# Kernel tuning notes

Hardware: AMD Instinct MI355X
Metric: run time of the kernel (lower is better)

## Reference

```python
import jax, jax.numpy as jnp
import numpy as np

B, S, D, F, E, SH, K = 2, 2048, 2048, 1024, 16, 2, 2


def setup_inputs() -> dict:
    key = jax.random.key(0)
    ks = jax.random.split(key, 8)
    std = 0.02
    mk = lambda k, sh: (jax.random.normal(k, sh, jnp.float32) * std)
    return {
        "x": jax.random.normal(ks[0], (B, S, D), jnp.float32),
        "wa": mk(ks[1], (D, E)),                      # router, no bias
        "rg": mk(ks[2], (E, D, F)), "rgb": jnp.zeros((E, F), jnp.float32),
        "rw1": mk(ks[3], (E, D, F)), "rb1": jnp.zeros((E, F), jnp.float32),
        "rw2": mk(ks[4], (E, F, D)), "rb2": jnp.zeros((E, D), jnp.float32),
        "sg": mk(ks[5], (SH, D, F)), "sgb": jnp.zeros((SH, F), jnp.float32),
        "sw1": mk(ks[6], (SH, D, F)), "sb1": jnp.zeros((SH, F), jnp.float32),
        "sw2": mk(ks[7], (SH, F, D)), "sb2": jnp.zeros((SH, D), jnp.float32),
    }


def _experts_all(x, g, gb, w1, b1, w2, b2):
    """Run every expert in the stack on every token.
    x: [b,s,d]; g,w1: [e,d,f]; w2: [e,f,d] -> out [b,s,e,d].
    Expert: w2( gelu(gated(x)) * w1(x) ). torch GELU default = exact erf.
    """
    y = jax.nn.gelu(jnp.einsum('bsd,edf->bsef', x, g) + gb, approximate=False)
    y = y * (jnp.einsum('bsd,edf->bsef', x, w1) + b1)
    return jnp.einsum('bsef,efd->bsed', y, w2) + b2


def reference(x, wa, rg, rgb, rw1, rb1, rw2, rb2, sg, sgb, sw1, sb1, sw2, sb2):
    # sigmoid affinity router + top-k, renormalized over the k selected
    aff = jax.nn.sigmoid(jnp.einsum('bsd,de->bse', x, wa))
    topk_p, topk_i = jax.lax.top_k(aff, K)                   # [b,s,k]
    topk_p = topk_p / jnp.sum(topk_p, axis=-1, keepdims=True)
    # dense combine weights [b,s,E]; zero for unselected experts, so the
    # masked-scatter of the original is reproduced exactly by a weighted sum
    combine = jnp.sum(jax.nn.one_hot(topk_i, E, dtype=x.dtype) * topk_p[..., None], axis=2)
    routed = jnp.einsum('bsed,bse->bsd',
                        _experts_all(x, rg, rgb, rw1, rb1, rw2, rb2), combine)
    shared = jnp.sum(_experts_all(x, sg, sgb, sw1, sb1, sw2, sb2), axis=2)
    return x + shared + routed
```

## Files before the change

kernel.cpp:

```cpp
#include <hip/hip_runtime.h>
#include <hip/hip_bf16.h>
#include <math.h>

typedef __bf16 bf16;
typedef bf16  bf16x8 __attribute__((ext_vector_type(8)));
typedef bf16  bf16x4 __attribute__((ext_vector_type(4)));
typedef float f32x4  __attribute__((ext_vector_type(4)));

#define TOKENS 4096
#define DM 2048
#define FF 1024
#define NE 16
#define SH_BASE 12288
#define BK 64

#define WS_CNT    0
#define WS_POS    64
#define WS_BASE   128
#define WS_TOPKW  256
#define WS_TOPKI  33024
#define WS_TSLOT  65792
#define WS_LIST   98560
#define WS_XB     180480
#define WS_H      16957696
#define WS_Y      58900736
#define WS_B1R    142786816
#define WS_B1S    277004544
#define WS_W2TR   293781760
#define WS_W2TS   360890624

__device__ __forceinline__ bf16 f2bf(float f) {
  unsigned u = __builtin_bit_cast(unsigned, f);
  u += 0x7fffu + ((u >> 16) & 1u);
  unsigned short h = (unsigned short)(u >> 16);
  return __builtin_bit_cast(bf16, h);
}

typedef const __attribute__((address_space(1))) void* gas_t;
typedef __attribute__((address_space(3))) void* las_t;
__device__ __forceinline__ void load_lds16(const bf16* g, bf16* l) {
  __builtin_amdgcn_global_load_lds((gas_t)g, (las_t)l, 16, 0, 0);
}

__global__ void cvt_x_kernel(const float* __restrict__ x, bf16* __restrict__ xb) {
  const size_t idx = ((size_t)blockIdx.x * 256 + threadIdx.x) * 4;
  f32x4 v = *(const f32x4*)(x + idx);
  bf16x4 o;
  o[0] = f2bf(v[0]); o[1] = f2bf(v[1]); o[2] = f2bf(v[2]); o[3] = f2bf(v[3]);
  *(bf16x4*)(xb + idx) = o;
}

__global__ void transpose_cvt_kernel(const float* __restrict__ in, bf16* __restrict__ out,
                                     int R, int C) {
  __shared__ float tile[64][65];
  const size_t zo = (size_t)blockIdx.z * R * C;
  const int c0 = blockIdx.x * 64, r0 = blockIdx.y * 64;
  const int t = threadIdx.x;
  const int tc = t & 63, tr = t >> 6;
#pragma unroll
  for (int i = 0; i < 16; i++) {
    const int r = tr * 16 + i;
    tile[r][tc] = in[zo + (size_t)(r0 + r) * C + c0 + tc];
  }
  __syncthreads();
  const int co = t >> 4;
  const int ro = (t & 15) * 4;
#pragma unroll
  for (int j = 0; j < 4; j++) {
    const int c = co + j * 16;
    bf16x4 v;
    v[0] = f2bf(tile[ro + 0][c]);
    v[1] = f2bf(tile[ro + 1][c]);
    v[2] = f2bf(tile[ro + 2][c]);
    v[3] = f2bf(tile[ro + 3][c]);
    *(bf16x4*)(out + zo + (size_t)(c0 + c) * R + r0 + ro) = v;
  }
}

__global__ void transpose_cvt_fused_kernel(const float* __restrict__ in, bf16* __restrict__ out,
                                           int half) {
  __shared__ float tile[64][65];
  const size_t zi = (size_t)blockIdx.z * DM * FF;
  const size_t zo = (size_t)blockIdx.z * (2 * FF) * DM;
  const int c0 = blockIdx.x * 64, r0 = blockIdx.y * 64;
  const int t = threadIdx.x;
  const int tc = t & 63, tr = t >> 6;
#pragma unroll
  for (int i = 0; i < 16; i++) {
    const int r = tr * 16 + i;
    tile[r][tc] = in[zi + (size_t)(r0 + r) * FF + c0 + tc];
  }
  __syncthreads();
  const int co = t >> 4;
  const int ro = (t & 15) * 4;
#pragma unroll
  for (int j = 0; j < 4; j++) {
    const int c = co + j * 16;
    const int f = c0 + c;
    const int fr = ((f >> 4) << 5) + half * 16 + (f & 15);
    bf16x4 v;
    v[0] = f2bf(tile[ro + 0][c]);
    v[1] = f2bf(tile[ro + 1][c]);
    v[2] = f2bf(tile[ro + 2][c]);
    v[3] = f2bf(tile[ro + 3][c]);
    *(bf16x4*)(out + zo + (size_t)fr * DM + r0 + ro) = v;
  }
}

#define RT_TOK 16
#define RT_DK  256
#define RT_PITCH (RT_DK + 4)

__global__ __launch_bounds__(256) void router_kernel(
    const float* __restrict__ x, const float* __restrict__ wa,
    float* __restrict__ topk_w, int* __restrict__ topk_i,
    int* __restrict__ cnt) {
  __shared__ float xs[RT_TOK][RT_PITCH];
  __shared__ float was[NE][RT_PITCH];
  __shared__ float aff[RT_TOK][17];

  const int tid = threadIdx.x;
  const int t = tid >> 4;
  const int e = tid & 15;
  const int t0 = blockIdx.x * RT_TOK;

  f32x4 acc4 = {0.f, 0.f, 0.f, 0.f};

  for (int d0 = 0; d0 < DM; d0 += RT_DK) {
    __syncthreads();
    {
      const int r = tid >> 4;
      const int c4 = (tid & 15) * 4;
      const float* src = x + (size_t)(t0 + r) * DM + d0;
#pragma unroll
      for (int j = 0; j < 4; j++)
        *(f32x4*)(&xs[r][c4 + j * 64]) = *(const f32x4*)(src + c4 + j * 64);
    }
    {
      const int e2 = tid & 15;
      const int dd = (tid >> 4) * 16;
#pragma unroll
      for (int j = 0; j < 16; j++)
        was[e2][dd + j] = wa[(size_t)(d0 + dd + j) * NE + e2];
    }
    __syncthreads();
#pragma unroll 16
    for (int d = 0; d < RT_DK; d += 4) {
      const f32x4 xv = *(const f32x4*)(&xs[t][d]);
      const f32x4 wv = *(const f32x4*)(&was[e][d]);
      acc4 += xv * wv;
    }
  }

  const float a = acc4[0] + acc4[1] + acc4[2] + acc4[3];
  aff[t][e] = 1.f / (1.f + expf(-a));
  __syncthreads();

  if (e == 0) {
    float b0 = -1e30f, b1 = -1e30f; int i0 = 0, i1 = 0;
    for (int i = 0; i < NE; i++) {
      const float v = aff[t][i];
      if (v > b0) { b1 = b0; i1 = i0; b0 = v; i0 = i; }
      else if (v > b1) { b1 = v; i1 = i; }
    }
    const int tok = t0 + t;
    const float inv = 1.f / (b0 + b1);
    topk_w[tok * 2] = b0 * inv;  topk_w[tok * 2 + 1] = b1 * inv;
    topk_i[tok * 2] = i0;        topk_i[tok * 2 + 1] = i1;
    atomicAdd(&cnt[i0], 1);      atomicAdd(&cnt[i1], 1);
  }
}

__global__ void prefix_kernel(const int* __restrict__ cnt, int* __restrict__ base) {
  if (threadIdx.x == 0) {
    int acc = 0;
    for (int e = 0; e < NE; e++) { base[e] = acc; acc += (cnt[e] + 127) & ~127; }
    base[NE] = SH_BASE;
    base[NE + 1] = SH_BASE + TOKENS;
  }
}

__global__ void build_lists_kernel(const int* __restrict__ topk_i, const int* __restrict__ base,
                                   int* __restrict__ pos, int* __restrict__ list,
                                   int* __restrict__ token_slot) {
  const int t = blockIdx.x * 256 + threadIdx.x;
  if (t >= TOKENS) return;
#pragma unroll
  for (int k = 0; k < 2; k++) {
    const int e = topk_i[t * 2 + k];
    const int p = atomicAdd(&pos[e], 1);
    const int slot = base[e] + p;
    list[slot] = t;
    token_slot[t * 2 + k] = slot;
  }
  list[SH_BASE + t] = t;
  list[SH_BASE + TOKENS + t] = t;
}

__global__ __launch_bounds__(256, 2) void gemm1_kernel(
    const bf16* __restrict__ xb, const int* __restrict__ list,
    const int* __restrict__ base, const int* __restrict__ cnt,
    const bf16* __restrict__ B1R, const bf16* __restrict__ B1S,
    const float* __restrict__ rgb, const float* __restrict__ rb1,
    const float* __restrict__ sgb, const float* __restrict__ sb1,
    bf16* __restrict__ H) {
  const int e = blockIdx.z;
  const int ce = (e < NE) ? cnt[e] : TOKENS;
  const int m0 = blockIdx.y * 128;
  if (m0 >= ce) return;
  const int n0 = blockIdx.x * 128;
  const int bse = base[e];

  const bf16* B1; const float *gb, *ub;
  if (e < NE) { B1 = B1R + (size_t)e * (2 * FF) * DM; gb = rgb + e * FF; ub = rb1 + e * FF; }
  else { const int s = e - NE; B1 = B1S + (size_t)s * (2 * FF) * DM; gb = sgb + s * FF; ub = sb1 + s * FF; }

  __shared__ bf16 As[2][128 * BK];
  __shared__ bf16 Bs[2][128 * BK];

  const int tid = threadIdx.x, lane = tid & 63, wid = tid >> 6;
  const int lrow = lane >> 3;
  const int laneK = (((lane & 7) ^ lrow) << 3);
  const int q0 = wid << 5;

  const bf16* aP[4];
#pragma unroll
  for (int i = 0; i < 4; i++) {
    int rA = m0 + q0 + (i << 3) + lrow;
    if (rA >= ce) rA = ce - 1;
    aP[i] = xb + (size_t)list[bse + rA] * DM + laneK;
  }
  const bf16* bP = B1 + (size_t)(n0 + q0 + lrow) * DM + laneK;

  const int wm = (wid & 1) * 64, wn = (wid >> 1) * 64;
  const int m16 = lane & 15, quad = lane >> 4, xor7 = m16 & 7;

  f32x4 acc[4][4] = {};

#pragma unroll
  for (int i = 0; i < 4; i++) {
    load_lds16(aP[i], &As[0][(q0 + (i << 3)) * BK + (lane << 3)]);
    load_lds16(bP + (size_t)(i * 8) * DM, &Bs[0][(q0 + (i << 3)) * BK + (lane << 3)]);
  }

  int cur = 0;
  for (int k0 = 0; k0 < DM; k0 += BK) {
    __syncthreads();
    if (k0 + BK < DM) {
      const int nxt = cur ^ 1;
      const int kn = k0 + BK;
#pragma unroll
      for (int i = 0; i < 4; i++) {
        load_lds16(aP[i] + kn, &As[nxt][(q0 + (i << 3)) * BK + (lane << 3)]);
        load_lds16(bP + (size_t)(i * 8) * DM + kn, &Bs[nxt][(q0 + (i << 3)) * BK + (lane << 3)]);
      }
    }
#pragma unroll
    for (int kk = 0; kk < 2; kk++) {
      const int slot = (((kk << 2) + quad) ^ xor7) << 3;
      bf16x8 af[4], bfr[4];
#pragma unroll
      for (int i = 0; i < 4; i++) {
        af[i]  = *(const bf16x8*)(&As[cur][(wm + m16 + 16 * i) * BK + slot]);
        bfr[i] = *(const bf16x8*)(&Bs[cur][(wn + m16 + 16 * i) * BK + slot]);
      }
#pragma unroll
      for (int mi = 0; mi < 4; mi++)
#pragma unroll
        for (int ni = 0; ni < 4; ni++)
          acc[mi][ni] = __builtin_amdgcn_mfma_f32_16x16x32_bf16(af[mi], bfr[ni], acc[mi][ni], 0, 0, 0);
    }
    cur ^= 1;
  }

  const int q4 = quad * 4;
  const int fbase = ((n0 + wn) >> 1) + m16;
#pragma unroll
  for (int mi = 0; mi < 4; mi++) {
#pragma unroll
    for (int nj = 0; nj < 2; nj++) {
      const int f = fbase + nj * 16;
      const float gbv = gb[f], ubv = ub[f];
#pragma unroll
      for (int r = 0; r < 4; r++) {
        const int row = m0 + wm + mi * 16 + q4 + r;
        const float g = acc[mi][2 * nj][r] + gbv;
        const float u = acc[mi][2 * nj + 1][r] + ubv;
        const float h = 0.5f * g * (1.f + erff(g * 0.70710678118f)) * u;
        H[(size_t)(bse + row) * FF + f] = f2bf(h);
      }
    }
  }
}

__global__ __launch_bounds__(256, 2) void gemm2_kernel(
    const bf16* __restrict__ Hb, const int* __restrict__ base, const int* __restrict__ cnt,
    const bf16* __restrict__ rw2T, const bf16* __restrict__ sw2T,
    const float* __restrict__ rb2, const float* __restrict__ sb2,
    bf16* __restrict__ Y) {
  const int e = blockIdx.z;
  const int ce = (e < NE) ? cnt[e] : TOKENS;
  const int m0 = blockIdx.y * 128;
  if (m0 >= ce) return;
  const int n0 = blockIdx.x * 128;
  const int bse = base[e];

  const bf16* B; const float* bb;
  if (e < NE) { B = rw2T + (size_t)e * DM * FF; bb = rb2 + e * DM; }
  else { const int s = e - NE; B = sw2T + (size_t)s * DM * FF; bb = sb2 + s * DM; }

  __shared__ bf16 As[2][128 * BK];
  __shared__ bf16 Bs[2][128 * BK];

  const int tid = threadIdx.x, lane = tid & 63, wid = tid >> 6;
  const int lrow = lane >> 3;
  const int laneK = (((lane & 7) ^ lrow) << 3);
  const int q0 = wid << 5;

  const bf16* aP = Hb + (size_t)(bse + m0 + q0 + lrow) * FF + laneK;
  const bf16* bP = B  + (size_t)(n0 + q0 + lrow) * FF + laneK;

  const int wm = (wid & 1) * 64, wn = (wid >> 1) * 64;
  const int m16 = lane & 15, quad = lane >> 4, xor7 = m16 & 7;

  f32x4 acc[4][4] = {};

#pragma unroll
  for (int i = 0; i < 4; i++) {
    load_lds16(aP + (size_t)(i * 8) * FF, &As[0][(q0 + (i << 3)) * BK + (lane << 3)]);
    load_lds16(bP + (size_t)(i * 8) * FF, &Bs[0][(q0 + (i << 3)) * BK + (lane << 3)]);
  }

  int cur = 0;
  for (int k0 = 0; k0 < FF; k0 += BK) {
    __syncthreads();
    if (k0 + BK < FF) {
      const int nxt = cur ^ 1;
      const int kn = k0 + BK;
#pragma unroll
      for (int i = 0; i < 4; i++) {
        load_lds16(aP + (size_t)(i * 8) * FF + kn, &As[nxt][(q0 + (i << 3)) * BK + (lane << 3)]);
        load_lds16(bP + (size_t)(i * 8) * FF + kn, &Bs[nxt][(q0 + (i << 3)) * BK + (lane << 3)]);
      }
    }
#pragma unroll
    for (int kk = 0; kk < 2; kk++) {
      const int slot = (((kk << 2) + quad) ^ xor7) << 3;
      bf16x8 af[4], bfr[4];
#pragma unroll
      for (int i = 0; i < 4; i++) {
        af[i]  = *(const bf16x8*)(&As[cur][(wm + m16 + 16 * i) * BK + slot]);
        bfr[i] = *(const bf16x8*)(&Bs[cur][(wn + m16 + 16 * i) * BK + slot]);
      }
#pragma unroll
      for (int mi = 0; mi < 4; mi++)
#pragma unroll
        for (int ni = 0; ni < 4; ni++)
          acc[mi][ni] = __builtin_amdgcn_mfma_f32_16x16x32_bf16(af[mi], bfr[ni], acc[mi][ni], 0, 0, 0);
    }
    cur ^= 1;
  }

  const int q4 = quad * 4;
#pragma unroll
  for (int mi = 0; mi < 4; mi++) {
#pragma unroll
    for (int ni = 0; ni < 4; ni++) {
      const int n = n0 + wn + ni * 16 + m16;
      const float bv = bb[n];
#pragma unroll
      for (int r = 0; r < 4; r++) {
        const int row = m0 + wm + mi * 16 + q4 + r;
        Y[(size_t)(bse + row) * DM + n] = f2bf(acc[mi][ni][r] + bv);
      }
    }
  }
}

__global__ void combine_kernel(const float* __restrict__ x, const bf16* __restrict__ Y,
                               const int* __restrict__ token_slot, const float* __restrict__ topk_w,
                               float* __restrict__ out) {
  const int t = blockIdx.x;
  const int d = threadIdx.x * 8;
  const int s0 = token_slot[t * 2], s1 = token_slot[t * 2 + 1];
  const float w0 = topk_w[t * 2], w1 = topk_w[t * 2 + 1];
  const bf16x8 ya = *(const bf16x8*)(Y + (size_t)(SH_BASE + t) * DM + d);
  const bf16x8 yb = *(const bf16x8*)(Y + (size_t)(SH_BASE + TOKENS + t) * DM + d);
  const bf16x8 y0 = *(const bf16x8*)(Y + (size_t)s0 * DM + d);
  const bf16x8 y1 = *(const bf16x8*)(Y + (size_t)s1 * DM + d);
  const float* xp = x + (size_t)t * DM + d;
  float* op = out + (size_t)t * DM + d;
#pragma unroll
  for (int j = 0; j < 8; j++)
    op[j] = xp[j] + (float)ya[j] + (float)yb[j] + w0 * (float)y0[j] + w1 * (float)y1[j];
}

extern "C" void kernel_launch(void* const* d_in, const int* in_sizes, int n_in,
                              void* d_out, int out_size, void* d_ws, size_t ws_size,
                              hipStream_t stream) {
  (void)in_sizes; (void)n_in; (void)out_size; (void)ws_size;
  const float* x   = (const float*)d_in[0];
  const float* wa  = (const float*)d_in[1];
  const float* rg  = (const float*)d_in[2];
  const float* rgb = (const float*)d_in[3];
  const float* rw1 = (const float*)d_in[4];
  const float* rb1 = (const float*)d_in[5];
  const float* rw2 = (const float*)d_in[6];
  const float* rb2 = (const float*)d_in[7];
  const float* sg  = (const float*)d_in[8];
  const float* sgb = (const float*)d_in[9];
  const float* sw1 = (const float*)d_in[10];
  const float* sb1 = (const float*)d_in[11];
  const float* sw2 = (const float*)d_in[12];
  const float* sb2 = (const float*)d_in[13];
  float* out = (float*)d_out;

  char* ws = (char*)d_ws;
  int*   cnt        = (int*)(ws + WS_CNT);
  int*   pos        = (int*)(ws + WS_POS);
  int*   basep      = (int*)(ws + WS_BASE);
  float* topk_w     = (float*)(ws + WS_TOPKW);
  int*   topk_i     = (int*)(ws + WS_TOPKI);
  int*   token_slot = (int*)(ws + WS_TSLOT);
  int*   list       = (int*)(ws + WS_LIST);
  bf16*  xb         = (bf16*)(ws + WS_XB);
  bf16*  H          = (bf16*)(ws + WS_H);
  bf16*  Y          = (bf16*)(ws + WS_Y);
  bf16*  B1R        = (bf16*)(ws + WS_B1R);
  bf16*  B1S        = (bf16*)(ws + WS_B1S);
  bf16*  W2TR       = (bf16*)(ws + WS_W2TR);
  bf16*  W2TS       = (bf16*)(ws + WS_W2TS);

  hipMemsetAsync(ws, 0, 128, stream);

  cvt_x_kernel<<<(TOKENS * DM) / 1024, 256, 0, stream>>>(x, xb);
  router_kernel<<<TOKENS / RT_TOK, 256, 0, stream>>>(x, wa, topk_w, topk_i, cnt);
  prefix_kernel<<<1, 64, 0, stream>>>(cnt, basep);
  build_lists_kernel<<<TOKENS / 256, 256, 0, stream>>>(topk_i, basep, pos, list, token_slot);

  transpose_cvt_fused_kernel<<<dim3(FF / 64, DM / 64, NE), 256, 0, stream>>>(rg,  B1R, 0);
  transpose_cvt_fused_kernel<<<dim3(FF / 64, DM / 64, NE), 256, 0, stream>>>(rw1, B1R, 1);
  transpose_cvt_fused_kernel<<<dim3(FF / 64, DM / 64, 2),  256, 0, stream>>>(sg,  B1S, 0);
  transpose_cvt_fused_kernel<<<dim3(FF / 64, DM / 64, 2),  256, 0, stream>>>(sw1, B1S, 1);
  transpose_cvt_kernel<<<dim3(DM / 64, FF / 64, NE), 256, 0, stream>>>(rw2, W2TR, FF, DM);
  transpose_cvt_kernel<<<dim3(DM / 64, FF / 64, 2),  256, 0, stream>>>(sw2, W2TS, FF, DM);

  gemm1_kernel<<<dim3((2 * FF) / 128, 32, 18), 256, 0, stream>>>(
      xb, list, basep, cnt, B1R, B1S, rgb, rb1, sgb, sb1, H);
  gemm2_kernel<<<dim3(DM / 128, 32, 18), 256, 0, stream>>>(
      H, basep, cnt, W2TR, W2TS, rb2, sb2, Y);
  combine_kernel<<<TOKENS, 256, 0, stream>>>(x, Y, token_slot, topk_w, out);
}
```

Baseline: 916.5 us.

## Enlarge expert GEMM tiles to 256x256 with four-stage LDS pipeline

Both grouped expert GEMMs move from 128x128 tiles with a double-buffered K=64 loop to 256x256 tiles over 512 threads. The K loop now uses K=32 steps with a four-buffer LDS ring, explicit vmcnt waits and raw barriers, plus s_setprio around the MFMA block. Expert slot padding grows to 256 rows to match the new M tile. The aim is more operand reuse per loaded byte and better hiding of load latency. In exchange, each block needs 128KB of LDS, so only one block fits per CU, and the larger tiles waste more work on partially filled expert tiles.

```diff
diff --git a/kernel.cpp b/kernel.cpp
--- a/kernel.cpp
+++ b/kernel.cpp
@@ -12,7 +12,6 @@
 #define FF 1024
 #define NE 16
 #define SH_BASE 12288
-#define BK 64
 
 #define WS_CNT    0
 #define WS_POS    64
@@ -174,7 +173,7 @@
 __global__ void prefix_kernel(const int* __restrict__ cnt, int* __restrict__ base) {
   if (threadIdx.x == 0) {
     int acc = 0;
-    for (int e = 0; e < NE; e++) { base[e] = acc; acc += (cnt[e] + 127) & ~127; }
+    for (int e = 0; e < NE; e++) { base[e] = acc; acc += (cnt[e] + 255) & ~255; }
     base[NE] = SH_BASE;
     base[NE + 1] = SH_BASE + TOKENS;
   }
@@ -197,7 +196,8 @@
   list[SH_BASE + TOKENS + t] = t;
 }
 
-__global__ __launch_bounds__(256, 2) void gemm1_kernel(
+
+__global__ __launch_bounds__(512, 2) void gemm1_kernel(
     const bf16* __restrict__ xb, const int* __restrict__ list,
     const int* __restrict__ base, const int* __restrict__ cnt,
     const bf16* __restrict__ B1R, const bf16* __restrict__ B1S,
@@ -206,77 +206,85 @@
     bf16* __restrict__ H) {
   const int e = blockIdx.z;
   const int ce = (e < NE) ? cnt[e] : TOKENS;
-  const int m0 = blockIdx.y * 128;
+  const int m0 = blockIdx.y * 256;
   if (m0 >= ce) return;
-  const int n0 = blockIdx.x * 128;
+  const int n0 = blockIdx.x * 256;
   const int bse = base[e];
 
   const bf16* B1; const float *gb, *ub;
   if (e < NE) { B1 = B1R + (size_t)e * (2 * FF) * DM; gb = rgb + e * FF; ub = rb1 + e * FF; }
   else { const int s = e - NE; B1 = B1S + (size_t)s * (2 * FF) * DM; gb = sgb + s * FF; ub = sb1 + s * FF; }
 
-  __shared__ bf16 As[2][128 * BK];
-  __shared__ bf16 Bs[2][128 * BK];
+  __shared__ bf16 As[4 * 8192];
+  __shared__ bf16 Bs[4 * 8192];
 
   const int tid = threadIdx.x, lane = tid & 63, wid = tid >> 6;
-  const int lrow = lane >> 3;
-  const int laneK = (((lane & 7) ^ lrow) << 3);
-  const int q0 = wid << 5;
-
-  const bf16* aP[4];
-#pragma unroll
-  for (int i = 0; i < 4; i++) {
-    int rA = m0 + q0 + (i << 3) + lrow;
-    if (rA >= ce) rA = ce - 1;
-    aP[i] = xb + (size_t)list[bse + rA] * DM + laneK;
-  }
-  const bf16* bP = B1 + (size_t)(n0 + q0 + lrow) * DM + laneK;
-
-  const int wm = (wid & 1) * 64, wn = (wid >> 1) * 64;
-  const int m16 = lane & 15, quad = lane >> 4, xor7 = m16 & 7;
-
-  f32x4 acc[4][4] = {};
-
-#pragma unroll
-  for (int i = 0; i < 4; i++) {
-    load_lds16(aP[i], &As[0][(q0 + (i << 3)) * BK + (lane << 3)]);
-    load_lds16(bP + (size_t)(i * 8) * DM, &Bs[0][(q0 + (i << 3)) * BK + (lane << 3)]);
-  }
-
-  int cur = 0;
-  for (int k0 = 0; k0 < DM; k0 += BK) {
-    __syncthreads();
-    if (k0 + BK < DM) {
-      const int nxt = cur ^ 1;
-      const int kn = k0 + BK;
-#pragma unroll
-      for (int i = 0; i < 4; i++) {
-        load_lds16(aP[i] + kn, &As[nxt][(q0 + (i << 3)) * BK + (lane << 3)]);
-        load_lds16(bP + (size_t)(i * 8) * DM + kn, &Bs[nxt][(q0 + (i << 3)) * BK + (lane << 3)]);
-      }
-    }
-#pragma unroll
-    for (int kk = 0; kk < 2; kk++) {
-      const int slot = (((kk << 2) + quad) ^ xor7) << 3;
-      bf16x8 af[4], bfr[4];
-#pragma unroll
-      for (int i = 0; i < 4; i++) {
-        af[i]  = *(const bf16x8*)(&As[cur][(wm + m16 + 16 * i) * BK + slot]);
-        bfr[i] = *(const bf16x8*)(&Bs[cur][(wn + m16 + 16 * i) * BK + slot]);
-      }
-#pragma unroll
-      for (int mi = 0; mi < 4; mi++)
-#pragma unroll
-        for (int ni = 0; ni < 4; ni++)
-          acc[mi][ni] = __builtin_amdgcn_mfma_f32_16x16x32_bf16(af[mi], bfr[ni], acc[mi][ni], 0, 0, 0);
-    }
-    cur ^= 1;
+  const int m16 = lane & 15, quad = lane >> 4;
+  const int wm = (wid & 1) * 128, wn = (wid >> 1) * 64;
+  const int rg8 = (quad ^ (m16 & 3)) << 3;
+
+  const int r0 = tid >> 2;
+  const int swz = ((tid & 3) ^ (r0 & 3)) << 3;
+  int ra0 = m0 + r0;       if (ra0 >= ce) ra0 = ce - 1;
+  int ra1 = m0 + 128 + r0; if (ra1 >= ce) ra1 = ce - 1;
+  const bf16* aSrc0 = xb + (size_t)list[bse + ra0] * DM + swz;
+  const bf16* aSrc1 = xb + (size_t)list[bse + ra1] * DM + swz;
+  const bf16* bSrc0 = B1 + (size_t)(n0 + r0) * DM + swz;
+  const bf16* bSrc1 = B1 + (size_t)(n0 + 128 + r0) * DM + swz;
+
+  f32x4 acc[8][4] = {};
+
+#pragma unroll
+  for (int t = 0; t < 3; t++) {
+    bf16* Ad = As + t * 8192; bf16* Bd = Bs + t * 8192;
+    const int k = t * 32;
+    load_lds16(aSrc0 + k, Ad + tid * 8);
+    load_lds16(aSrc1 + k, Ad + 4096 + tid * 8);
+    load_lds16(bSrc0 + k, Bd + tid * 8);
+    load_lds16(bSrc1 + k, Bd + 4096 + tid * 8);
+  }
+  asm volatile("s_waitcnt vmcnt(8)" ::: "memory");
+  __builtin_amdgcn_s_barrier();
+
+  const int NT = DM / 32;
+  for (int t = 0; t < NT; ++t) {
+    if (t + 3 < NT) {
+      const int sb = (t + 3) & 3;
+      bf16* Ad = As + sb * 8192; bf16* Bd = Bs + sb * 8192;
+      const int k = (t + 3) * 32;
+      load_lds16(aSrc0 + k, Ad + tid * 8);
+      load_lds16(aSrc1 + k, Ad + 4096 + tid * 8);
+      load_lds16(bSrc0 + k, Bd + tid * 8);
+      load_lds16(bSrc1 + k, Bd + 4096 + tid * 8);
+    }
+    {
+      const bf16* Ab = As + (t & 3) * 8192;
+      const bf16* Bb = Bs + (t & 3) * 8192;
+      bf16x8 af[8], bv[4];
+#pragma unroll
+      for (int i = 0; i < 8; i++)
+        af[i] = *(const bf16x8*)(Ab + (wm + 16 * i + m16) * 32 + rg8);
+#pragma unroll
+      for (int j = 0; j < 4; j++)
+        bv[j] = *(const bf16x8*)(Bb + (wn + 16 * j + m16) * 32 + rg8);
+      __builtin_amdgcn_s_setprio(1);
+#pragma unroll
+      for (int i = 0; i < 8; i++)
+#pragma unroll
+        for (int j = 0; j < 4; j++)
+          acc[i][j] = __builtin_amdgcn_mfma_f32_16x16x32_bf16(af[i], bv[j], acc[i][j], 0, 0, 0);
+      __builtin_amdgcn_s_setprio(0);
+    }
+    if (t < NT - 3)       asm volatile("s_waitcnt vmcnt(8)" ::: "memory");
+    else if (t == NT - 3) asm volatile("s_waitcnt vmcnt(4)" ::: "memory");
+    else if (t == NT - 2) asm volatile("s_waitcnt vmcnt(0)" ::: "memory");
+    if (t < NT - 1) __builtin_amdgcn_s_barrier();
   }
 
   const int q4 = quad * 4;
   const int fbase = ((n0 + wn) >> 1) + m16;
 #pragma unroll
-  for (int mi = 0; mi < 4; mi++) {
+  for (int mi = 0; mi < 8; mi++) {
 #pragma unroll
     for (int nj = 0; nj < 2; nj++) {
       const int f = fbase + nj * 16;
@@ -293,85 +301,97 @@
   }
 }
 
-__global__ __launch_bounds__(256, 2) void gemm2_kernel(
+__global__ __launch_bounds__(512, 2) void gemm2_kernel(
     const bf16* __restrict__ Hb, const int* __restrict__ base, const int* __restrict__ cnt,
     const bf16* __restrict__ rw2T, const bf16* __restrict__ sw2T,
     const float* __restrict__ rb2, const float* __restrict__ sb2,
     bf16* __restrict__ Y) {
   const int e = blockIdx.z;
   const int ce = (e < NE) ? cnt[e] : TOKENS;
-  const int m0 = blockIdx.y * 128;
+  const int m0 = blockIdx.y * 256;
   if (m0 >= ce) return;
-  const int n0 = blockIdx.x * 128;
+  const int n0 = blockIdx.x * 256;
   const int bse = base[e];
 
   const bf16* B; const float* bb;
   if (e < NE) { B = rw2T + (size_t)e * DM * FF; bb = rb2 + e * DM; }
   else { const int s = e - NE; B = sw2T + (size_t)s * DM * FF; bb = sb2 + s * DM; }
 
-  __shared__ bf16 As[2][128 * BK];
-  __shared__ bf16 Bs[2][128 * BK];
+  __shared__ bf16 As[4 * 8192];
+  __shared__ bf16 Bs[4 * 8192];
 
   const int tid = threadIdx.x, lane = tid & 63, wid = tid >> 6;
-  const int lrow = lane >> 3;
-  const int laneK = (((lane & 7) ^ lrow) << 3);
-  const int q0 = wid << 5;
-
-  const bf16* aP = Hb + (size_t)(bse + m0 + q0 + lrow) * FF + laneK;
-  const bf16* bP = B  + (size_t)(n0 + q0 + lrow) * FF + laneK;
-
-  const int wm = (wid & 1) * 64, wn = (wid >> 1) * 64;
-  const int m16 = lane & 15, quad = lane >> 4, xor7 = m16 & 7;
-
-  f32x4 acc[4][4] = {};
-
-#pragma unroll
-  for (int i = 0; i < 4; i++) {
-    load_lds16(aP + (size_t)(i * 8) * FF, &As[0][(q0 + (i << 3)) * BK + (lane << 3)]);
-    load_lds16(bP + (size_t)(i * 8) * FF, &Bs[0][(q0 + (i << 3)) * BK + (lane << 3)]);
-  }
-
-  int cur = 0;
-  for (int k0 = 0; k0 < FF; k0 += BK) {
-    __syncthreads();
-    if (k0 + BK < FF) {
-      const int nxt = cur ^ 1;
-      const int kn = k0 + BK;
-#pragma unroll
-      for (int i = 0; i < 4; i++) {
-        load_lds16(aP + (size_t)(i * 8) * FF + kn, &As[nxt][(q0 + (i << 3)) * BK + (lane << 3)]);
-        load_lds16(bP + (size_t)(i * 8) * FF + kn, &Bs[nxt][(q0 + (i << 3)) * BK + (lane << 3)]);
-      }
-    }
-#pragma unroll
-    for (int kk = 0; kk < 2; kk++) {
-      const int slot = (((kk << 2) + quad) ^ xor7) << 3;
-      bf16x8 af[4], bfr[4];
-#pragma unroll
-      for (int i = 0; i < 4; i++) {
-        af[i]  = *(const bf16x8*)(&As[cur][(wm + m16 + 16 * i) * BK + slot]);
-        bfr[i] = *(const bf16x8*)(&Bs[cur][(wn + m16 + 16 * i) * BK + slot]);
-      }
-#pragma unroll
-      for (int mi = 0; mi < 4; mi++)
-#pragma unroll
-        for (int ni = 0; ni < 4; ni++)
-          acc[mi][ni] = __builtin_amdgcn_mfma_f32_16x16x32_bf16(af[mi], bfr[ni], acc[mi][ni], 0, 0, 0);
-    }
-    cur ^= 1;
+  const int m16 = lane & 15, quad = lane >> 4;
+  const int wm = (wid & 1) * 128, wn = (wid >> 1) * 64;
+  const int rg8 = (quad ^ (m16 & 3)) << 3;
+
+  const int r0 = tid >> 2;
+  const int swz = ((tid & 3) ^ (r0 & 3)) << 3;
+  const bf16* aSrc0 = Hb + (size_t)(bse + m0 + r0) * FF + swz;
+  const bf16* aSrc1 = Hb + (size_t)(bse + m0 + 128 + r0) * FF + swz;
+  const bf16* bSrc0 = B + (size_t)(n0 + r0) * FF + swz;
+  const bf16* bSrc1 = B + (size_t)(n0 + 128 + r0) * FF + swz;
+
+  f32x4 acc[8][4] = {};
+
+#pragma unroll
+  for (int t = 0; t < 3; t++) {
+    bf16* Ad = As + t * 8192; bf16* Bd = Bs + t * 8192;
+    const int k = t * 32;
+    load_lds16(aSrc0 + k, Ad + tid * 8);
+    load_lds16(aSrc1 + k, Ad + 4096 + tid * 8);
+    load_lds16(bSrc0 + k, Bd + tid * 8);
+    load_lds16(bSrc1 + k, Bd + 4096 + tid * 8);
+  }
+  asm volatile("s_waitcnt vmcnt(8)" ::: "memory");
+  __builtin_amdgcn_s_barrier();
+
+  const int NT = FF / 32;
+  for (int t = 0; t < NT; ++t) {
+    if (t + 3 < NT) {
+      const int sb = (t + 3) & 3;
+      bf16* Ad = As + sb * 8192; bf16* Bd = Bs + sb * 8192;
+      const int k = (t + 3) * 32;
+      load_lds16(aSrc0 + k, Ad + tid * 8);
+      load_lds16(aSrc1 + k, Ad + 4096 + tid * 8);
+      load_lds16(bSrc0 + k, Bd + tid * 8);
+      load_lds16(bSrc1 + k, Bd + 4096 + tid * 8);
+    }
+    {
+      const bf16* Ab = As + (t & 3) * 8192;
+      const bf16* Bb = Bs + (t & 3) * 8192;
+      bf16x8 af[8], bv[4];
+#pragma unroll
+      for (int i = 0; i < 8; i++)
+        af[i] = *(const bf16x8*)(Ab + (wm + 16 * i + m16) * 32 + rg8);
+#pragma unroll
+      for (int j = 0; j < 4; j++)
+        bv[j] = *(const bf16x8*)(Bb + (wn + 16 * j + m16) * 32 + rg8);
+      __builtin_amdgcn_s_setprio(1);
+#pragma unroll
+      for (int i = 0; i < 8; i++)
+#pragma unroll
+        for (int j = 0; j < 4; j++)
+          acc[i][j] = __builtin_amdgcn_mfma_f32_16x16x32_bf16(af[i], bv[j], acc[i][j], 0, 0, 0);
+      __builtin_amdgcn_s_setprio(0);
+    }
+    if (t < NT - 3)       asm volatile("s_waitcnt vmcnt(8)" ::: "memory");
+    else if (t == NT - 3) asm volatile("s_waitcnt vmcnt(4)" ::: "memory");
+    else if (t == NT - 2) asm volatile("s_waitcnt vmcnt(0)" ::: "memory");
+    if (t < NT - 1) __builtin_amdgcn_s_barrier();
   }
 
   const int q4 = quad * 4;
 #pragma unroll
-  for (int mi = 0; mi < 4; mi++) {
+  for (int mi = 0; mi < 8; mi++) {
 #pragma unroll
     for (int ni = 0; ni < 4; ni++) {
       const int n = n0 + wn + ni * 16 + m16;
-      const float bv = bb[n];
+      const float bv2 = bb[n];
 #pragma unroll
       for (int r = 0; r < 4; r++) {
         const int row = m0 + wm + mi * 16 + q4 + r;
-        Y[(size_t)(bse + row) * DM + n] = f2bf(acc[mi][ni][r] + bv);
+        Y[(size_t)(bse + row) * DM + n] = f2bf(acc[mi][ni][r] + bv2);
       }
     }
   }
@@ -445,9 +465,9 @@
   transpose_cvt_kernel<<<dim3(DM / 64, FF / 64, NE), 256, 0, stream>>>(rw2, W2TR, FF, DM);
   transpose_cvt_kernel<<<dim3(DM / 64, FF / 64, 2),  256, 0, stream>>>(sw2, W2TS, FF, DM);
 
-  gemm1_kernel<<<dim3((2 * FF) / 128, 32, 18), 256, 0, stream>>>(
+  gemm1_kernel<<<dim3((2 * FF) / 256, 16, 18), 512, 0, stream>>>(
       xb, list, basep, cnt, B1R, B1S, rgb, rb1, sgb, sb1, H);
-  gemm2_kernel<<<dim3(DM / 128, 32, 18), 256, 0, stream>>>(
+  gemm2_kernel<<<dim3(DM / 256, 16, 18), 512, 0, stream>>>(
       H, basep, cnt, W2TR, W2TS, rb2, sb2, Y);
   combine_kernel<<<TOKENS, 256, 0, stream>>>(x, Y, token_slot, topk_w, out);
 }
```

New measurement: 1.024 ms. +11.8%, slower.

## Remap GEMM blocks per XCD for L2 reuse and vectorize transpose loads

Applied to the files above, without the earlier changes.

The GEMM kernels now launch on a flat 1-D grid and remap the block index so that consecutive tiles of the same expert and row block land on the same XCD. This aims to improve L2 reuse of weights and activations across the MI355X's chiplets. Separately, the transpose/convert kernels now read float4 vectors per thread instead of scalar loads, which cuts load instruction count. The remap assumes a grid divisible by 8 and that the hardware dispatches blocks round-robin across XCDs; it also adds a small amount of index arithmetic per block.

```diff
diff --git a/kernel.cpp b/kernel.cpp
--- a/kernel.cpp
+++ b/kernel.cpp
@@ -56,11 +56,16 @@
   const size_t zo = (size_t)blockIdx.z * R * C;
   const int c0 = blockIdx.x * 64, r0 = blockIdx.y * 64;
   const int t = threadIdx.x;
-  const int tc = t & 63, tr = t >> 6;
-#pragma unroll
-  for (int i = 0; i < 16; i++) {
-    const int r = tr * 16 + i;
-    tile[r][tc] = in[zo + (size_t)(r0 + r) * C + c0 + tc];
+  const int lr = t >> 2;
+  const int lc = (t & 3) * 4;
+  const float* src = in + zo + (size_t)(r0 + lr) * C + c0;
+#pragma unroll
+  for (int j = 0; j < 4; j++) {
+    const f32x4 v = *(const f32x4*)(src + lc + j * 16);
+    tile[lr][lc + j * 16 + 0] = v[0];
+    tile[lr][lc + j * 16 + 1] = v[1];
+    tile[lr][lc + j * 16 + 2] = v[2];
+    tile[lr][lc + j * 16 + 3] = v[3];
   }
   __syncthreads();
   const int co = t >> 4;
@@ -84,11 +89,16 @@
   const size_t zo = (size_t)blockIdx.z * (2 * FF) * DM;
   const int c0 = blockIdx.x * 64, r0 = blockIdx.y * 64;
   const int t = threadIdx.x;
-  const int tc = t & 63, tr = t >> 6;
-#pragma unroll
-  for (int i = 0; i < 16; i++) {
-    const int r = tr * 16 + i;
-    tile[r][tc] = in[zi + (size_t)(r0 + r) * FF + c0 + tc];
+  const int lr = t >> 2;
+  const int lc = (t & 3) * 4;
+  const float* src = in + zi + (size_t)(r0 + lr) * FF + c0;
+#pragma unroll
+  for (int j = 0; j < 4; j++) {
+    const f32x4 v = *(const f32x4*)(src + lc + j * 16);
+    tile[lr][lc + j * 16 + 0] = v[0];
+    tile[lr][lc + j * 16 + 1] = v[1];
+    tile[lr][lc + j * 16 + 2] = v[2];
+    tile[lr][lc + j * 16 + 3] = v[3];
   }
   __syncthreads();
   const int co = t >> 4;
@@ -197,6 +207,18 @@
   list[SH_BASE + TOKENS + t] = t;
 }
 
+#define G1_NX 16
+#define G1_MY 32
+#define G1_EZ 18
+#define GEMM_GRID (G1_NX * G1_MY * G1_EZ)
+
+__device__ __forceinline__ void xcd_tile(int flat, int nx_dim, int& nx, int& my, int& ez) {
+  const int s = (flat & 7) * (GEMM_GRID / 8) + (flat >> 3);
+  nx = s % nx_dim;
+  my = (s / nx_dim) & 31;
+  ez = s / (nx_dim * 32);
+}
+
 __global__ __launch_bounds__(256, 2) void gemm1_kernel(
     const bf16* __restrict__ xb, const int* __restrict__ list,
     const int* __restrict__ base, const int* __restrict__ cnt,
@@ -204,11 +226,12 @@
     const float* __restrict__ rgb, const float* __restrict__ rb1,
     const float* __restrict__ sgb, const float* __restrict__ sb1,
     bf16* __restrict__ H) {
-  const int e = blockIdx.z;
+  int bnx, bmy, e;
+  xcd_tile(blockIdx.x, G1_NX, bnx, bmy, e);
   const int ce = (e < NE) ? cnt[e] : TOKENS;
-  const int m0 = blockIdx.y * 128;
+  const int m0 = bmy * 128;
   if (m0 >= ce) return;
-  const int n0 = blockIdx.x * 128;
+  const int n0 = bnx * 128;
   const int bse = base[e];
 
   const bf16* B1; const float *gb, *ub;
@@ -298,11 +321,12 @@
     const bf16* __restrict__ rw2T, const bf16* __restrict__ sw2T,
     const float* __restrict__ rb2, const float* __restrict__ sb2,
     bf16* __restrict__ Y) {
-  const int e = blockIdx.z;
+  int bnx, bmy, e;
+  xcd_tile(blockIdx.x, DM / 128, bnx, bmy, e);
   const int ce = (e < NE) ? cnt[e] : TOKENS;
-  const int m0 = blockIdx.y * 128;
+  const int m0 = bmy * 128;
   if (m0 >= ce) return;
-  const int n0 = blockIdx.x * 128;
+  const int n0 = bnx * 128;
   const int bse = base[e];
 
   const bf16* B; const float* bb;
@@ -445,9 +469,9 @@
   transpose_cvt_kernel<<<dim3(DM / 64, FF / 64, NE), 256, 0, stream>>>(rw2, W2TR, FF, DM);
   transpose_cvt_kernel<<<dim3(DM / 64, FF / 64, 2),  256, 0, stream>>>(sw2, W2TS, FF, DM);
 
-  gemm1_kernel<<<dim3((2 * FF) / 128, 32, 18), 256, 0, stream>>>(
+  gemm1_kernel<<<GEMM_GRID, 256, 0, stream>>>(
       xb, list, basep, cnt, B1R, B1S, rgb, rb1, sgb, sb1, H);
-  gemm2_kernel<<<dim3(DM / 128, 32, 18), 256, 0, stream>>>(
+  gemm2_kernel<<<GEMM_GRID, 256, 0, stream>>>(
       H, basep, cnt, W2TR, W2TS, rb2, sb2, Y);
   combine_kernel<<<TOKENS, 256, 0, stream>>>(x, Y, token_slot, topk_w, out);
 }
```

After: 1.540 ms. 1.68x slower.
